# Optimization experiments

Measured on AMD Instinct MI355X. Metric: run time of the kernel, lower is better.

Reference implementation:

```python
import jax, jax.numpy as jnp
import numpy as np

B, N, IN_DIM, D, H, L = 4, 2048, 1, 256, 8, 4
DH = D // H          # 32 head dim
ROPE_D = DH // 2     # 16 = rotary dim per spatial axis (relative_emb_dim=2)
MIN_FREQ_SCALE = 64.0  # scale / min_freq = 1.0 / (1/64)
EPS = 1e-5


def setup_inputs():
    key = jax.random.key(0)
    ks = jax.random.split(key, 12)
    s = 0.02
    return {
        'h': jax.random.normal(ks[0], (B, N, IN_DIM), jnp.float32),
        'pos': jax.random.uniform(ks[1], (B, N, 2), jnp.float32),
        'proj_w': jax.random.normal(ks[2], (IN_DIM, D), jnp.float32) * s,
        'proj_b': jnp.zeros((D,), jnp.float32),
        'qkv_w': jax.random.normal(ks[3], (L, D, 3 * D), jnp.float32) * s,
        'out_w': jax.random.normal(ks[4], (L, D, D), jnp.float32) * s,
        'out_b': jnp.zeros((L, D), jnp.float32),
        'O_w': jax.random.normal(ks[5], (L, D, D), jnp.float32) * s,
        'O_b': jnp.zeros((L, D), jnp.float32),
        'ffn1_w': jax.random.normal(ks[6], (L, D, 2 * D), jnp.float32) * s,
        'ffn1_b': jnp.zeros((L, 2 * D), jnp.float32),
        'ffn2_w': jax.random.normal(ks[7], (L, 2 * D, D), jnp.float32) * s,
        'ffn2_b': jnp.zeros((L, D), jnp.float32),
        'ln1_g': jnp.ones((L, D), jnp.float32),
        'ln1_b': jnp.zeros((L, D), jnp.float32),
        'ln2_g': jnp.ones((L, D), jnp.float32),
        'ln2_b': jnp.zeros((L, D), jnp.float32),
        'final_w': jax.random.normal(ks[8], (D, D), jnp.float32) * s,
    }


def _rope_freqs(coords):
    # coords: (B, N) -> freqs (B, N, ROPE_D)
    inv_freq = 1.0 / (10000.0 ** (jnp.arange(0, ROPE_D, 2, dtype=jnp.float32) / ROPE_D))
    f = (coords * MIN_FREQ_SCALE)[..., None] * inv_freq
    return jnp.concatenate([f, f], axis=-1)


def _rotate_half(x):
    d = x.shape[-1] // 2
    return jnp.concatenate([-x[..., d:], x[..., :d]], axis=-1)


def _apply_rope(t, f):
    return t * jnp.cos(f) + _rotate_half(t) * jnp.sin(f)


def _apply_2d_rope(t, ft, fx):
    d = t.shape[-1] // 2
    return jnp.concatenate([_apply_rope(t[..., :d], ft), _apply_rope(t[..., d:], fx)], axis=-1)


def _ln(x, g, b):
    m = jnp.mean(x, -1, keepdims=True)
    v = jnp.mean((x - m) ** 2, -1, keepdims=True)
    return (x - m) / jnp.sqrt(v + EPS) * g + b


def _forward(h, pos, proj_w, proj_b, qkv_w, out_w, out_b, O_w, O_b,
             ffn1_w, ffn1_b, ffn2_w, ffn2_b, ln1_g, ln1_b, ln2_g, ln2_b, final_w):
    h = h @ proj_w + proj_b                      # (B, N, D)
    ft = _rope_freqs(pos[..., 0])[:, None]       # (B, 1, N, ROPE_D) broadcast over heads
    fx = _rope_freqs(pos[..., 1])[:, None]
    scale = DH ** -0.5
    for l in range(L):
        qkv = h @ qkv_w[l]                       # (B, N, 3D)
        q, k, v = jnp.split(qkv, 3, axis=-1)
        to_heads = lambda t: t.reshape(B, N, H, DH).transpose(0, 2, 1, 3)
        q, k, v = to_heads(q), to_heads(k), to_heads(v)
        q = _apply_2d_rope(q, ft, fx)
        k = _apply_2d_rope(k, ft, fx)
        attn = jax.nn.softmax(jnp.einsum('bhid,bhjd->bhij', q, k) * scale, axis=-1)
        o = jnp.einsum('bhij,bhjd->bhid', attn, v)
        o = o.transpose(0, 2, 1, 3).reshape(B, N, D)
        o = o @ out_w[l] + out_b[l]              # attention to_out
        o = o @ O_w[l] + O_b[l]                  # layer O projection
        h = _ln(h + o, ln1_g[l], ln1_b[l])
        f = jax.nn.relu(h @ ffn1_w[l] + ffn1_b[l]) @ ffn2_w[l] + ffn2_b[l]
        h = _ln(h + f, ln2_g[l], ln2_b[l])
    return h @ final_w


def reference(h, pos, proj_w, proj_b, qkv_w, out_w, out_b, O_w, O_b,
              ffn1_w, ffn1_b, ffn2_w, ffn2_b, ln1_g, ln1_b, ln2_g, ln2_b, final_w):
    return _forward(h, pos, proj_w, proj_b, qkv_w, out_w, out_b, O_w, O_b,
                    ffn1_w, ffn1_b, ffn2_w, ffn2_b, ln1_g, ln1_b, ln2_g, ln2_b, final_w)
```

## Files before the change

### kernel.cpp

```cpp
#include <hip/hip_runtime.h>
#include <math.h>

#define B_ 4
#define N_ 2048
#define D_ 256
#define H_ 8
#define L_ 4
#define DH_ 32

typedef float f32x4 __attribute__((ext_vector_type(4)));
typedef float f32x16 __attribute__((ext_vector_type(16)));
typedef short short8 __attribute__((ext_vector_type(8)));
typedef unsigned short ushort_t;
typedef ushort_t ushortx4 __attribute__((ext_vector_type(4)));
typedef ushort_t ushortx8 __attribute__((ext_vector_type(8)));

typedef __attribute__((address_space(3))) unsigned int lds_u32_t;
typedef __attribute__((address_space(1))) unsigned int glb_u32_t;

static __device__ __forceinline__ ushort_t f2bf(float x) {
    unsigned int u = __float_as_uint(x);
    unsigned int r = (u + 0x7fffu + ((u >> 16) & 1u)) >> 16;
    return (ushort_t)r;
}

static __device__ __forceinline__ unsigned int cvt_pk_bf16(float a, float b) {
    unsigned int w;
    asm("v_cvt_pk_bf16_f32 %0, %1, %2" : "=v"(w) : "v"(a), "v"(b));
    return w;
}

static __device__ __forceinline__ float xhalf_max(float x) {
    unsigned int a = __float_as_uint(x), b = a;
    asm volatile("v_permlane32_swap_b32 %0, %1" : "+v"(a), "+v"(b));
    return fmaxf(__uint_as_float(a), __uint_as_float(b));
}
static __device__ __forceinline__ float xhalf_add(float x) {
    unsigned int a = __float_as_uint(x), b = a;
    asm volatile("v_permlane32_swap_b32 %0, %1" : "+v"(a), "+v"(b));
    return __uint_as_float(a) + __uint_as_float(b);
}

__global__ __launch_bounds__(256) void proj_kernel(
    const float* __restrict__ hin, const float* __restrict__ w,
    const float* __restrict__ bias, float* __restrict__ hout,
    ushort_t* __restrict__ hb)
{
    long idx = (long)blockIdx.x * 256 + threadIdx.x;
    long bn = idx >> 6;
    int d4 = (int)(idx & 63) << 2;
    float hv = hin[bn];
    float4 wv = *(const float4*)&w[d4];
    float4 bv = *(const float4*)&bias[d4];
    float4 o;
    o.x = hv * wv.x + bv.x;
    o.y = hv * wv.y + bv.y;
    o.z = hv * wv.z + bv.z;
    o.w = hv * wv.w + bv.w;
    *(float4*)&hout[bn * D_ + d4] = o;
    ushortx4 ob;
    ob[0] = f2bf(o.x); ob[1] = f2bf(o.y); ob[2] = f2bf(o.z); ob[3] = f2bf(o.w);
    *(ushortx4*)&hb[bn * D_ + d4] = ob;
}

__global__ __launch_bounds__(256) void rope_table_kernel(
    const float* __restrict__ pos, float* __restrict__ tab)
{
    int i = blockIdx.x * 256 + threadIdx.x;
    if (i >= B_ * N_) return;
    float t = pos[i * 2 + 0] * 64.0f;
    float x = pos[i * 2 + 1] * 64.0f;
    float* o = tab + (long)i * 32;
    const float log2_1e4_over8 = 13.28771237954945f / 8.0f;
    #pragma unroll
    for (int j = 0; j < 8; ++j) {
        float invf = exp2f(-(float)j * log2_1e4_over8);
        float st, ct, sx, cx;
        sincosf(t * invf, &st, &ct);
        sincosf(x * invf, &sx, &cx);
        o[j]      = ct;
        o[8 + j]  = st;
        o[16 + j] = cx;
        o[24 + j] = sx;
    }
}

__global__ __launch_bounds__(256) void prep_qkv(
    const float* __restrict__ qkv, const float* __restrict__ tab,
    ushort_t* __restrict__ Qb, ushort_t* __restrict__ Kb, ushort_t* __restrict__ Vt)
{
    const float F = 0.17677669529663687f * 1.4426950408889634f;
    int bh = blockIdx.y;
    int b = bh >> 3, h = bh & 7;
    int n0 = blockIdx.x << 6;
    int t = threadIdx.x;

    #pragma unroll
    for (int i = 0; i < 4; ++i) {
        int item = t + (i << 8);
        int tok = item >> 4, p = item & 15;
        long bn = (long)b * N_ + n0 + tok;
        int half = p >> 3, j = p & 7;
        const float* tb = tab + bn * 32;
        float c = tb[half * 16 + j];
        float s = tb[half * 16 + 8 + j];
        float cF = c * F, sF = s * F;
        long obase = ((long)bh * N_ + n0 + tok) * DH_;
        const float* base = qkv + bn * (3 * D_) + h * DH_ + half * 16 + j;
        int d0 = half * 16 + j;
        float q0 = base[0], q1 = base[8];
        Qb[obase + d0]     = f2bf(q0 * cF - q1 * sF);
        Qb[obase + d0 + 8] = f2bf(q1 * cF + q0 * sF);
        float k0 = base[D_], k1 = base[D_ + 8];
        Kb[obase + d0]     = f2bf(k0 * c - k1 * s);
        Kb[obase + d0 + 8] = f2bf(k1 * c + k0 * s);
    }

    __shared__ float T[64][36];
    int r = t >> 2, c0 = (t & 3) << 3;
    const float* src = qkv + ((long)b * N_ + n0 + r) * (3 * D_) + 2 * D_ + h * DH_ + c0;
    float4 a = ((const float4*)src)[0];
    float4 bb = ((const float4*)src)[1];
    *(float4*)&T[r][c0] = a;
    *(float4*)&T[r][c0 + 4] = bb;
    __syncthreads();
    int d = t >> 3, n8 = (t & 7) << 3;
    ushortx8 o;
    #pragma unroll
    for (int i = 0; i < 8; ++i) o[i] = f2bf(T[n8 + i][d]);
    *(ushortx8*)&Vt[((long)bh * DH_ + d) * N_ + n0 + n8] = o;
}

__global__ __launch_bounds__(256) void wprep_kernel(
    const float* __restrict__ qkv_w, const float* __restrict__ out_w,
    const float* __restrict__ O_w, const float* __restrict__ ffn1_w,
    const float* __restrict__ ffn2_w, const float* __restrict__ final_w,
    ushort_t* __restrict__ WT)
{
    int bid = blockIdx.x;
    const float* src; ushort_t* dst; int K, Nn, tile;
    if (bid < 192)      { int l = bid / 48;        tile = bid % 48;        src = qkv_w  + (long)l * 196608; dst = WT + (long)l * 196608;           K = 256; Nn = 768; }
    else if (bid < 256) { int r = bid - 192; int l = r / 16; tile = r % 16; src = out_w  + (long)l * 65536;  dst = WT + 786432  + (long)l * 65536;  K = 256; Nn = 256; }
    else if (bid < 320) { int r = bid - 256; int l = r / 16; tile = r % 16; src = O_w    + (long)l * 65536;  dst = WT + 1048576 + (long)l * 65536;  K = 256; Nn = 256; }
    else if (bid < 448) { int r = bid - 320; int l = r / 32; tile = r % 32; src = ffn1_w + (long)l * 131072; dst = WT + 1310720 + (long)l * 131072; K = 256; Nn = 512; }
    else if (bid < 576) { int r = bid - 448; int l = r / 32; tile = r % 32; src = ffn2_w + (long)l * 131072; dst = WT + 1835008 + (long)l * 131072; K = 512; Nn = 256; }
    else                { tile = bid - 576;                                 src = final_w;                   dst = WT + 2359296;                    K = 256; Nn = 256; }
    int ntn = Nn >> 6;
    int kt = (tile / ntn) << 6;
    int nt = (tile % ntn) << 6;
    __shared__ float Tl[64][65];
    int t = threadIdx.x;
    int kr = t >> 2, nc0 = (t & 3) << 4;
    const float* sp = src + (long)(kt + kr) * Nn + nt + nc0;
    float4 v0 = ((const float4*)sp)[0];
    float4 v1 = ((const float4*)sp)[1];
    float4 v2 = ((const float4*)sp)[2];
    float4 v3 = ((const float4*)sp)[3];
    float* tr = &Tl[kr][nc0];
    tr[0] = v0.x; tr[1] = v0.y; tr[2] = v0.z; tr[3] = v0.w;
    tr[4] = v1.x; tr[5] = v1.y; tr[6] = v1.z; tr[7] = v1.w;
    tr[8] = v2.x; tr[9] = v2.y; tr[10] = v2.z; tr[11] = v2.w;
    tr[12] = v3.x; tr[13] = v3.y; tr[14] = v3.z; tr[15] = v3.w;
    __syncthreads();
    int n = t >> 2, kc0 = (t & 3) << 4;
    ushortx8 o0, o1;
    #pragma unroll
    for (int i = 0; i < 8; ++i) o0[i] = f2bf(Tl[kc0 + i][n]);
    #pragma unroll
    for (int i = 0; i < 8; ++i) o1[i] = f2bf(Tl[kc0 + 8 + i][n]);
    ushort_t* dp = dst + (long)(nt + n) * K + kt + kc0;
    *(ushortx8*)dp = o0;
    *(ushortx8*)(dp + 8) = o1;
}

__global__ __launch_bounds__(256) void wfold_kernel(
    const float* __restrict__ out_w, const float* __restrict__ O_w,
    ushort_t* __restrict__ WTp)
{
    int l = blockIdx.x >> 4;
    int t4 = blockIdx.x & 15;
    int k0 = (t4 >> 2) << 6, n0 = (t4 & 3) << 6;
    const float* Am = out_w + (long)l * 65536;
    const float* Bm = O_w + (long)l * 65536;
    ushort_t* dst = WTp + (long)l * 65536;
    __shared__ float sA[16][68];
    __shared__ float sB[16][64];
    int tid = threadIdx.x;
    int tx = tid & 15, ty = tid >> 4;
    int arow = tid >> 2, acol = (tid & 3) << 2;
    int brow = tid >> 4, bcol = (tid & 15) << 2;
    const float* Aptr = Am + (long)(k0 + arow) * 256 + acol;
    const float* Bptr = Bm + (long)brow * 256 + n0 + bcol;
    float acc[4][4] = {{0.f}};
    for (int jt = 0; jt < 256; jt += 16) {
        float4 av = *(const float4*)(Aptr + jt);
        float4 bv = *(const float4*)(Bptr + (long)jt * 256);
        __syncthreads();
        sA[acol + 0][arow] = av.x;
        sA[acol + 1][arow] = av.y;
        sA[acol + 2][arow] = av.z;
        sA[acol + 3][arow] = av.w;
        *(float4*)&sB[brow][bcol] = bv;
        __syncthreads();
        #pragma unroll
        for (int kk = 0; kk < 16; ++kk) {
            float4 a = *(const float4*)&sA[kk][ty << 2];
            float4 b = *(const float4*)&sB[kk][tx << 2];
            acc[0][0] += a.x * b.x; acc[0][1] += a.x * b.y; acc[0][2] += a.x * b.z; acc[0][3] += a.x * b.w;
            acc[1][0] += a.y * b.x; acc[1][1] += a.y * b.y; acc[1][2] += a.y * b.z; acc[1][3] += a.y * b.w;
            acc[2][0] += a.z * b.x; acc[2][1] += a.z * b.y; acc[2][2] += a.z * b.z; acc[2][3] += a.z * b.w;
            acc[3][0] += a.w * b.x; acc[3][1] += a.w * b.y; acc[3][2] += a.w * b.z; acc[3][3] += a.w * b.w;
        }
    }
    #pragma unroll
    for (int i = 0; i < 4; ++i) {
        int k = k0 + (ty << 2) + i;
        #pragma unroll
        for (int c = 0; c < 4; ++c) {
            int n = n0 + (tx << 2) + c;
            dst[(long)n * 256 + k] = f2bf(acc[i][c]);
        }
    }
}

__global__ __launch_bounds__(256) void bfold_kernel(
    const float* __restrict__ out_b, const float* __restrict__ O_w,
    const float* __restrict__ O_b, float* __restrict__ bp)
{
    int l = blockIdx.x >> 3;
    int n = ((blockIdx.x & 7) << 5) + (threadIdx.x & 31);
    int jg = threadIdx.x >> 5;
    const float* Bm = O_w + (long)l * 65536;
    float acc = 0.f;
    #pragma unroll 8
    for (int j = jg * 32; j < jg * 32 + 32; ++j)
        acc += out_b[l * 256 + j] * Bm[(long)j * 256 + n];
    __shared__ float red[8][32];
    red[jg][threadIdx.x & 31] = acc;
    __syncthreads();
    if (threadIdx.x < 32) {
        int nn = ((blockIdx.x & 7) << 5) + threadIdx.x;
        float s = O_b[l * 256 + nn];
        #pragma unroll
        for (int g = 0; g < 8; ++g) s += red[g][threadIdx.x];
        bp[l * 256 + nn] = s;
    }
}

__global__ __launch_bounds__(256) void gemm_mfma2(
    const ushort_t* __restrict__ A, const ushort_t* __restrict__ BT,
    const float* __restrict__ bias, void* __restrict__ Cout,
    int N, int K, int flags)
{
    __shared__ ushort_t sA[2][8192];
    __shared__ ushort_t sB[2][4096];
    int tid = threadIdx.x;
    int wid = tid >> 6, lane = tid & 63;
    int lo = lane & 15, hi = lane >> 4;
    int wm = wid >> 1, wn = wid & 1;
    int m0 = blockIdx.y << 7, n0 = blockIdx.x << 6;

    int lrow = lane >> 3;
    int slot = lane & 7;
    const ushort_t* Ag[4];
    const ushort_t* Bg[2];
    #pragma unroll
    for (int c = 0; c < 4; ++c) {
        int arow = (wid << 5) + (c << 3) + lrow;
        Ag[c] = A + (long)(m0 + arow) * K + ((slot ^ lrow) << 3);
    }
    #pragma unroll
    for (int c = 0; c < 2; ++c) {
        int brow = (wid << 4) + (c << 3) + lrow;
        Bg[c] = BT + (long)(n0 + brow) * K + ((slot ^ lrow) << 3);
    }

#define STAGE(buf, koff) do { \
    _Pragma("unroll") \
    for (int c = 0; c < 4; ++c) \
        __builtin_amdgcn_global_load_lds((const glb_u32_t*)(Ag[c] + (koff)), \
            (lds_u32_t*)&sA[buf][((wid << 5) + (c << 3)) << 6], 16, 0, 0); \
    _Pragma("unroll") \
    for (int c = 0; c < 2; ++c) \
        __builtin_amdgcn_global_load_lds((const glb_u32_t*)(Bg[c] + (koff)), \
            (lds_u32_t*)&sB[buf][((wid << 4) + (c << 3)) << 6], 16, 0, 0); \
} while (0)

    f32x4 acc[4][2];
    #pragma unroll
    for (int i = 0; i < 4; ++i)
        #pragma unroll
        for (int j = 0; j < 2; ++j) acc[i][j] = (f32x4){0.f, 0.f, 0.f, 0.f};

    int ar[4], br[2];
    #pragma unroll
    for (int mf = 0; mf < 4; ++mf) ar[mf] = ((wm << 6) + (mf << 4) + lo) << 6;
    #pragma unroll
    for (int nf = 0; nf < 2; ++nf) br[nf] = ((wn << 5) + (nf << 4) + lo) << 6;
    int swz = lo & 7;

    int nk = K >> 6;
    STAGE(0, 0);
    for (int s = 0; s < nk; ++s) {
        int buf = s & 1;
        if (s + 1 < nk) {
            STAGE(buf ^ 1, (s + 1) << 6);
            asm volatile("s_waitcnt vmcnt(6)" ::: "memory");
        } else {
            asm volatile("s_waitcnt vmcnt(0)" ::: "memory");
        }
        __builtin_amdgcn_s_barrier();
        asm volatile("" ::: "memory");
        #pragma unroll
        for (int ks = 0; ks < 2; ++ks) {
            int ko = (((ks << 2) + hi) ^ swz) << 3;
            short8 a0 = *(const short8*)&sA[buf][ar[0] + ko];
            short8 a1 = *(const short8*)&sA[buf][ar[1] + ko];
            short8 a2 = *(const short8*)&sA[buf][ar[2] + ko];
            short8 a3 = *(const short8*)&sA[buf][ar[3] + ko];
            short8 b0 = *(const short8*)&sB[buf][br[0] + ko];
            short8 b1 = *(const short8*)&sB[buf][br[1] + ko];
            acc[0][0] = __builtin_amdgcn_mfma_f32_16x16x32_bf16(a0, b0, acc[0][0], 0, 0, 0);
            acc[0][1] = __builtin_amdgcn_mfma_f32_16x16x32_bf16(a0, b1, acc[0][1], 0, 0, 0);
            acc[1][0] = __builtin_amdgcn_mfma_f32_16x16x32_bf16(a1, b0, acc[1][0], 0, 0, 0);
            acc[1][1] = __builtin_amdgcn_mfma_f32_16x16x32_bf16(a1, b1, acc[1][1], 0, 0, 0);
            acc[2][0] = __builtin_amdgcn_mfma_f32_16x16x32_bf16(a2, b0, acc[2][0], 0, 0, 0);
            acc[2][1] = __builtin_amdgcn_mfma_f32_16x16x32_bf16(a2, b1, acc[2][1], 0, 0, 0);
            acc[3][0] = __builtin_amdgcn_mfma_f32_16x16x32_bf16(a3, b0, acc[3][0], 0, 0, 0);
            acc[3][1] = __builtin_amdgcn_mfma_f32_16x16x32_bf16(a3, b1, acc[3][1], 0, 0, 0);
        }
        asm volatile("" ::: "memory");
        __builtin_amdgcn_s_barrier();
    }
#undef STAGE

    #pragma unroll
    for (int nf = 0; nf < 2; ++nf) {
        int col = n0 + (wn << 5) + (nf << 4) + lo;
        float bv = (flags & 1) ? bias[col] : 0.f;
        #pragma unroll
        for (int mf = 0; mf < 4; ++mf) {
            #pragma unroll
            for (int j = 0; j < 4; ++j) {
                float v = acc[mf][nf][j] + bv;
                if (flags & 2) v = fmaxf(v, 0.f);
                long row = m0 + (wm << 6) + (mf << 4) + (hi << 2) + j;
                if (flags & 4) ((ushort_t*)Cout)[row * N + col] = f2bf(v);
                else           ((float*)Cout)[row * N + col] = v;
            }
        }
    }
}

static __device__ __forceinline__ void attn_tile(
    short8 K00, short8 K01, short8 K10, short8 K11,
    short8 V00, short8 V01, short8 V10, short8 V11,
    short8 qf0, short8 qf1, int half, const f32x16& Z,
    float& m, float& lsum, f32x16& acc)
{
    f32x16 sa = __builtin_amdgcn_mfma_f32_32x32x16_bf16(K00, qf0, Z, 0, 0, 0);
    sa = __builtin_amdgcn_mfma_f32_32x32x16_bf16(K01, qf1, sa, 0, 0, 0);
    f32x16 sb = __builtin_amdgcn_mfma_f32_32x32x16_bf16(K10, qf0, Z, 0, 0, 0);
    sb = __builtin_amdgcn_mfma_f32_32x32x16_bf16(K11, qf1, sb, 0, 0, 0);

    float mx[16];
    #pragma unroll
    for (int r = 0; r < 16; ++r) mx[r] = fmaxf(sa[r], sb[r]);
    #pragma unroll
    for (int st = 8; st >= 1; st >>= 1) {
        #pragma unroll
        for (int r = 0; r < st; ++r) mx[r] = fmaxf(mx[r], mx[r + st]);
    }
    float pmax = xhalf_max(mx[0]);

    if (!__all(pmax <= m + 8.f)) {
        float mn = fmaxf(m, pmax);
        float corr = __builtin_amdgcn_exp2f(m - mn);
        m = mn; lsum *= corr;
        #pragma unroll
        for (int r = 0; r < 16; ++r) {
            int qr = (r & 3) + 8 * (r >> 2) + 4 * half;
            acc[r] *= __shfl(corr, qr, 64);
        }
    }

    float sm[16];
    #pragma unroll
    for (int r = 0; r < 16; ++r) {
        sa[r] = __builtin_amdgcn_exp2f(sa[r] - m);
        sb[r] = __builtin_amdgcn_exp2f(sb[r] - m);
        sm[r] = sa[r] + sb[r];
    }
    #pragma unroll
    for (int st = 8; st >= 1; st >>= 1) {
        #pragma unroll
        for (int r = 0; r < st; ++r) sm[r] += sm[r + st];
    }
    lsum += xhalf_add(sm[0]);

    unsigned int a0 = cvt_pk_bf16(sa[0], sa[1]),   a1 = cvt_pk_bf16(sa[2], sa[3]);
    unsigned int a2 = cvt_pk_bf16(sa[4], sa[5]),   a3 = cvt_pk_bf16(sa[6], sa[7]);
    unsigned int a4 = cvt_pk_bf16(sa[8], sa[9]),   a5 = cvt_pk_bf16(sa[10], sa[11]);
    unsigned int a6 = cvt_pk_bf16(sa[12], sa[13]), a7 = cvt_pk_bf16(sa[14], sa[15]);
    unsigned int b0 = cvt_pk_bf16(sb[0], sb[1]),   b1 = cvt_pk_bf16(sb[2], sb[3]);
    unsigned int b2 = cvt_pk_bf16(sb[4], sb[5]),   b3 = cvt_pk_bf16(sb[6], sb[7]);
    unsigned int b4 = cvt_pk_bf16(sb[8], sb[9]),   b5 = cvt_pk_bf16(sb[10], sb[11]);
    unsigned int b6 = cvt_pk_bf16(sb[12], sb[13]), b7 = cvt_pk_bf16(sb[14], sb[15]);
    asm volatile("v_permlane32_swap_b32 %0, %1" : "+v"(a0), "+v"(a2));
    asm volatile("v_permlane32_swap_b32 %0, %1" : "+v"(a1), "+v"(a3));
    asm volatile("v_permlane32_swap_b32 %0, %1" : "+v"(a4), "+v"(a6));
    asm volatile("v_permlane32_swap_b32 %0, %1" : "+v"(a5), "+v"(a7));
    asm volatile("v_permlane32_swap_b32 %0, %1" : "+v"(b0), "+v"(b2));
    asm volatile("v_permlane32_swap_b32 %0, %1" : "+v"(b1), "+v"(b3));
    asm volatile("v_permlane32_swap_b32 %0, %1" : "+v"(b4), "+v"(b6));
    asm volatile("v_permlane32_swap_b32 %0, %1" : "+v"(b5), "+v"(b7));
    union { unsigned int u[4]; short8 s8; } p0, p1, p2, p3;
    p0.u[0] = a0; p0.u[1] = a1; p0.u[2] = a2; p0.u[3] = a3;
    p1.u[0] = a4; p1.u[1] = a5; p1.u[2] = a6; p1.u[3] = a7;
    p2.u[0] = b0; p2.u[1] = b1; p2.u[2] = b2; p2.u[3] = b3;
    p3.u[0] = b4; p3.u[1] = b5; p3.u[2] = b6; p3.u[3] = b7;
    acc = __builtin_amdgcn_mfma_f32_32x32x16_bf16(p0.s8, V00, acc, 0, 0, 0);
    acc = __builtin_amdgcn_mfma_f32_32x32x16_bf16(p1.s8, V01, acc, 0, 0, 0);
    acc = __builtin_amdgcn_mfma_f32_32x32x16_bf16(p2.s8, V10, acc, 0, 0, 0);
    acc = __builtin_amdgcn_mfma_f32_32x32x16_bf16(p3.s8, V11, acc, 0, 0, 0);
}

__global__ __launch_bounds__(256) void attn_mfma4(
    const ushort_t* __restrict__ Qb, const ushort_t* __restrict__ Kb,
    const ushort_t* __restrict__ Vt, ushort_t* __restrict__ o)
{
    int bh = blockIdx.y;
    int tid = threadIdx.x;
    int wid = tid >> 6, lane = tid & 63;
    int lq = lane & 31;
    int half = lane >> 5;
    int qbase = (blockIdx.x << 7) + wid * 32;

    const ushort_t* Qp = Qb + (long)bh * N_ * DH_;
    const ushort_t* kp = Kb + (long)bh * N_ * DH_ + lq * DH_ + half * 8;
    const ushort_t* vp = Vt + (long)bh * DH_ * N_ + (long)lq * N_ + half * 8;

    short8 qf0 = *(const short8*)&Qp[(long)(qbase + lq) * DH_ + half * 8];
    short8 qf1 = *(const short8*)&Qp[(long)(qbase + lq) * DH_ + 16 + half * 8];

    f32x16 acc, Z;
    #pragma unroll
    for (int r = 0; r < 16; ++r) { acc[r] = 0.f; Z[r] = 0.f; }
    float m = -1e30f, lsum = 0.f;

    short8 k00 = *(const short8*)(kp +  0 * DH_);
    short8 k01 = *(const short8*)(kp +  0 * DH_ + 16);
    short8 k10 = *(const short8*)(kp + 32 * DH_);
    short8 k11 = *(const short8*)(kp + 32 * DH_ + 16);
    short8 v00 = *(const short8*)(vp +  0);
    short8 v01 = *(const short8*)(vp + 16);
    short8 v10 = *(const short8*)(vp + 32);
    short8 v11 = *(const short8*)(vp + 48);

    for (int it = 0; it < N_ / 64 - 1; ++it) {
        long kn = (long)(it + 1) << 6;
        short8 nk00 = *(const short8*)(kp + (kn +  0) * DH_);
        short8 nk01 = *(const short8*)(kp + (kn +  0) * DH_ + 16);
        short8 nk10 = *(const short8*)(kp + (kn + 32) * DH_);
        short8 nk11 = *(const short8*)(kp + (kn + 32) * DH_ + 16);
        short8 nv00 = *(const short8*)(vp + kn);
        short8 nv01 = *(const short8*)(vp + kn + 16);
        short8 nv10 = *(const short8*)(vp + kn + 32);
        short8 nv11 = *(const short8*)(vp + kn + 48);
        attn_tile(k00, k01, k10, k11, v00, v01, v10, v11, qf0, qf1, half, Z, m, lsum, acc);
        k00 = nk00; k01 = nk01; k10 = nk10; k11 = nk11;
        v00 = nv00; v01 = nv01; v10 = nv10; v11 = nv11;
    }
    attn_tile(k00, k01, k10, k11, v00, v01, v10, v11, qf0, qf1, half, Z, m, lsum, acc);

    float invl = 1.f / lsum;
    int b = bh >> 3, h = bh & 7;
    #pragma unroll
    for (int r = 0; r < 16; ++r) {
        int qr = (r & 3) + 8 * (r >> 2) + 4 * half;
        float iv = __shfl(invl, qr, 64);
        long row = (long)b * N_ + qbase + qr;
        o[row * D_ + h * DH_ + lq] = f2bf(acc[r] * iv);
    }
}

__global__ __launch_bounds__(256) void add_ln_kernel(
    float* __restrict__ h, const float* __restrict__ r,
    const float* __restrict__ g, const float* __restrict__ be,
    ushort_t* __restrict__ hb)
{
    int row = blockIdx.x * 4 + (threadIdx.x >> 6);
    int lane = threadIdx.x & 63;
    long off = (long)row * D_ + (lane << 2);
    float4 x = *(float4*)&h[off];
    float4 rr = *(const float4*)&r[off];
    x.x += rr.x; x.y += rr.y; x.z += rr.z; x.w += rr.w;
    float s = x.x + x.y + x.z + x.w;
    #pragma unroll
    for (int k = 1; k < 64; k <<= 1) s += __shfl_xor(s, k, 64);
    float mean = s * (1.f / 256.f);
    float dx = x.x - mean, dy = x.y - mean, dz = x.z - mean, dw = x.w - mean;
    float sq = dx * dx + dy * dy + dz * dz + dw * dw;
    #pragma unroll
    for (int k = 1; k < 64; k <<= 1) sq += __shfl_xor(sq, k, 64);
    float rstd = rsqrtf(sq * (1.f / 256.f) + 1e-5f);
    float4 gv = *(const float4*)&g[lane << 2];
    float4 bv = *(const float4*)&be[lane << 2];
    float4 o;
    o.x = dx * rstd * gv.x + bv.x;
    o.y = dy * rstd * gv.y + bv.y;
    o.z = dz * rstd * gv.z + bv.z;
    o.w = dw * rstd * gv.w + bv.w;
    *(float4*)&h[off] = o;
    ushortx4 ob;
    ob[0] = f2bf(o.x); ob[1] = f2bf(o.y); ob[2] = f2bf(o.z); ob[3] = f2bf(o.w);
    *(ushortx4*)&hb[off] = ob;
}

extern "C" void kernel_launch(void* const* d_in, const int* in_sizes, int n_in,
                              void* d_out, int out_size, void* d_ws, size_t ws_size,
                              hipStream_t stream) {
    const float* h_in    = (const float*)d_in[0];
    const float* pos     = (const float*)d_in[1];
    const float* proj_w  = (const float*)d_in[2];
    const float* proj_b  = (const float*)d_in[3];
    const float* qkv_w   = (const float*)d_in[4];
    const float* out_w   = (const float*)d_in[5];
    const float* out_b   = (const float*)d_in[6];
    const float* O_w     = (const float*)d_in[7];
    const float* O_b     = (const float*)d_in[8];
    const float* ffn1_w  = (const float*)d_in[9];
    const float* ffn1_b  = (const float*)d_in[10];
    const float* ffn2_w  = (const float*)d_in[11];
    const float* ffn2_b  = (const float*)d_in[12];
    const float* ln1_g   = (const float*)d_in[13];
    const float* ln1_b   = (const float*)d_in[14];
    const float* ln2_g   = (const float*)d_in[15];
    const float* ln2_b   = (const float*)d_in[16];
    const float* final_w = (const float*)d_in[17];
    float* out = (float*)d_out;

    float* ws   = (float*)d_ws;
    float* h    = ws;
    float* hb_f = h + 2097152;
    float* tab  = hb_f + 1048576;
    float* WT_f = tab + 262144;
    float* R    = WT_f + 1212416;
    float* QKV  = R + 6291456;
    float* tf   = QKV + 3145728;

    ushort_t* hb  = (ushort_t*)hb_f;
    ushort_t* WT  = (ushort_t*)WT_f;
    float*    qkvf = R;
    ushort_t* aob = (ushort_t*)R;
    ushort_t* fb  = (ushort_t*)(R + 2097152);
    float*    tf32 = R + 4194304;
    ushort_t* Qb  = (ushort_t*)QKV;
    ushort_t* Kb  = Qb + 2097152;
    ushort_t* Vtg = Kb + 2097152;
    ushort_t* WTp = (ushort_t*)tf;
    float*    bp  = tf + 131072;

    const long qkvT_off  = 0;
    const long ffn1T_off = 1310720;
    const long ffn2T_off = 1835008;
    const long finT_off  = 2359296;

    const long M = (long)B_ * N_;

    wprep_kernel<<<592, 256, 0, stream>>>(qkv_w, out_w, O_w, ffn1_w, ffn2_w, final_w, WT);
    wfold_kernel<<<64, 256, 0, stream>>>(out_w, O_w, WTp);
    bfold_kernel<<<32, 256, 0, stream>>>(out_b, O_w, O_b, bp);
    proj_kernel<<<(M * 64) / 256, 256, 0, stream>>>(h_in, proj_w, proj_b, h, hb);
    rope_table_kernel<<<(B_ * N_) / 256, 256, 0, stream>>>(pos, tab);

    for (int l = 0; l < L_; ++l) {
        gemm_mfma2<<<dim3(768 / 64, M / 128), 256, 0, stream>>>(
            hb, WT + qkvT_off + (long)l * 196608, nullptr, qkvf, 768, 256, 0);
        prep_qkv<<<dim3(N_ / 64, B_ * H_), 256, 0, stream>>>(qkvf, tab, Qb, Kb, Vtg);
        attn_mfma4<<<dim3(N_ / 128, B_ * H_), 256, 0, stream>>>(Qb, Kb, Vtg, aob);
        gemm_mfma2<<<dim3(256 / 64, M / 128), 256, 0, stream>>>(
            aob, WTp + (long)l * 65536, bp + (long)l * 256, tf32, 256, 256, 1);
        add_ln_kernel<<<M / 4, 256, 0, stream>>>(
            h, tf32, ln1_g + (long)l * D_, ln1_b + (long)l * D_, hb);
        gemm_mfma2<<<dim3(512 / 64, M / 128), 256, 0, stream>>>(
            hb, WT + ffn1T_off + (long)l * 131072, ffn1_b + (long)l * 2 * D_, fb, 512, 256, 1 | 2 | 4);
        gemm_mfma2<<<dim3(256 / 64, M / 128), 256, 0, stream>>>(
            fb, WT + ffn2T_off + (long)l * 131072, ffn2_b + (long)l * D_, tf32, 256, 512, 1);
        add_ln_kernel<<<M / 4, 256, 0, stream>>>(
            h, tf32, ln2_g + (long)l * D_, ln2_b + (long)l * D_, hb);
    }
    gemm_mfma2<<<dim3(256 / 64, M / 128), 256, 0, stream>>>(
        hb, WT + finT_off, nullptr, out, 256, 256, 0);
}
```

Baseline: 551.4 us.

## Split attention KV range in two with separate combine kernel

Attention now splits the key/value sequence into two halves, each handled by its own block, which doubles the grid from 512 to 1024 blocks to fill more compute units. Each split writes unnormalized fp32 partial outputs plus running max and sum, and a new combine kernel merges them into the bf16 output. The inner tile shrinks from 64 to 32 keys with no register prefetch, and occupancy is hinted through launch_bounds. In exchange it adds fp32 partial-result traffic, an extra kernel launch per layer, and less latency hiding inside the loop.

```diff
diff --git a/kernel.cpp b/kernel.cpp
--- a/kernel.cpp
+++ b/kernel.cpp
@@ -352,22 +352,19 @@
     }
 }
 
-static __device__ __forceinline__ void attn_tile(
-    short8 K00, short8 K01, short8 K10, short8 K11,
-    short8 V00, short8 V01, short8 V10, short8 V11,
+static __device__ __forceinline__ void attn_tile32(
+    short8 kf0, short8 kf1, short8 vb0, short8 vb1,
     short8 qf0, short8 qf1, int half, const f32x16& Z,
     float& m, float& lsum, f32x16& acc)
 {
-    f32x16 sa = __builtin_amdgcn_mfma_f32_32x32x16_bf16(K00, qf0, Z, 0, 0, 0);
-    sa = __builtin_amdgcn_mfma_f32_32x32x16_bf16(K01, qf1, sa, 0, 0, 0);
-    f32x16 sb = __builtin_amdgcn_mfma_f32_32x32x16_bf16(K10, qf0, Z, 0, 0, 0);
-    sb = __builtin_amdgcn_mfma_f32_32x32x16_bf16(K11, qf1, sb, 0, 0, 0);
-
-    float mx[16];
-    #pragma unroll
-    for (int r = 0; r < 16; ++r) mx[r] = fmaxf(sa[r], sb[r]);
-    #pragma unroll
-    for (int st = 8; st >= 1; st >>= 1) {
+    f32x16 sa = __builtin_amdgcn_mfma_f32_32x32x16_bf16(kf0, qf0, Z, 0, 0, 0);
+    sa = __builtin_amdgcn_mfma_f32_32x32x16_bf16(kf1, qf1, sa, 0, 0, 0);
+
+    float mx[8];
+    #pragma unroll
+    for (int r = 0; r < 8; ++r) mx[r] = fmaxf(sa[r], sa[r + 8]);
+    #pragma unroll
+    for (int st = 4; st >= 1; st >>= 1) {
         #pragma unroll
         for (int r = 0; r < st; ++r) mx[r] = fmaxf(mx[r], mx[r + st]);
     }
@@ -384,15 +381,13 @@
         }
     }
 
-    float sm[16];
-    #pragma unroll
-    for (int r = 0; r < 16; ++r) {
-        sa[r] = __builtin_amdgcn_exp2f(sa[r] - m);
-        sb[r] = __builtin_amdgcn_exp2f(sb[r] - m);
-        sm[r] = sa[r] + sb[r];
-    }
-    #pragma unroll
-    for (int st = 8; st >= 1; st >>= 1) {
+    float sm[8];
+    #pragma unroll
+    for (int r = 0; r < 16; ++r) sa[r] = __builtin_amdgcn_exp2f(sa[r] - m);
+    #pragma unroll
+    for (int r = 0; r < 8; ++r) sm[r] = sa[r] + sa[r + 8];
+    #pragma unroll
+    for (int st = 4; st >= 1; st >>= 1) {
         #pragma unroll
         for (int r = 0; r < st; ++r) sm[r] += sm[r + st];
     }
@@ -402,43 +397,33 @@
     unsigned int a2 = cvt_pk_bf16(sa[4], sa[5]),   a3 = cvt_pk_bf16(sa[6], sa[7]);
     unsigned int a4 = cvt_pk_bf16(sa[8], sa[9]),   a5 = cvt_pk_bf16(sa[10], sa[11]);
     unsigned int a6 = cvt_pk_bf16(sa[12], sa[13]), a7 = cvt_pk_bf16(sa[14], sa[15]);
-    unsigned int b0 = cvt_pk_bf16(sb[0], sb[1]),   b1 = cvt_pk_bf16(sb[2], sb[3]);
-    unsigned int b2 = cvt_pk_bf16(sb[4], sb[5]),   b3 = cvt_pk_bf16(sb[6], sb[7]);
-    unsigned int b4 = cvt_pk_bf16(sb[8], sb[9]),   b5 = cvt_pk_bf16(sb[10], sb[11]);
-    unsigned int b6 = cvt_pk_bf16(sb[12], sb[13]), b7 = cvt_pk_bf16(sb[14], sb[15]);
     asm volatile("v_permlane32_swap_b32 %0, %1" : "+v"(a0), "+v"(a2));
     asm volatile("v_permlane32_swap_b32 %0, %1" : "+v"(a1), "+v"(a3));
     asm volatile("v_permlane32_swap_b32 %0, %1" : "+v"(a4), "+v"(a6));
     asm volatile("v_permlane32_swap_b32 %0, %1" : "+v"(a5), "+v"(a7));
-    asm volatile("v_permlane32_swap_b32 %0, %1" : "+v"(b0), "+v"(b2));
-    asm volatile("v_permlane32_swap_b32 %0, %1" : "+v"(b1), "+v"(b3));
-    asm volatile("v_permlane32_swap_b32 %0, %1" : "+v"(b4), "+v"(b6));
-    asm volatile("v_permlane32_swap_b32 %0, %1" : "+v"(b5), "+v"(b7));
-    union { unsigned int u[4]; short8 s8; } p0, p1, p2, p3;
+    union { unsigned int u[4]; short8 s8; } p0, p1;
     p0.u[0] = a0; p0.u[1] = a1; p0.u[2] = a2; p0.u[3] = a3;
     p1.u[0] = a4; p1.u[1] = a5; p1.u[2] = a6; p1.u[3] = a7;
-    p2.u[0] = b0; p2.u[1] = b1; p2.u[2] = b2; p2.u[3] = b3;
-    p3.u[0] = b4; p3.u[1] = b5; p3.u[2] = b6; p3.u[3] = b7;
-    acc = __builtin_amdgcn_mfma_f32_32x32x16_bf16(p0.s8, V00, acc, 0, 0, 0);
-    acc = __builtin_amdgcn_mfma_f32_32x32x16_bf16(p1.s8, V01, acc, 0, 0, 0);
-    acc = __builtin_amdgcn_mfma_f32_32x32x16_bf16(p2.s8, V10, acc, 0, 0, 0);
-    acc = __builtin_amdgcn_mfma_f32_32x32x16_bf16(p3.s8, V11, acc, 0, 0, 0);
-}
-
-__global__ __launch_bounds__(256) void attn_mfma4(
+    acc = __builtin_amdgcn_mfma_f32_32x32x16_bf16(p0.s8, vb0, acc, 0, 0, 0);
+    acc = __builtin_amdgcn_mfma_f32_32x32x16_bf16(p1.s8, vb1, acc, 0, 0, 0);
+}
+
+__global__ __launch_bounds__(256, 4) void attn_split2(
     const ushort_t* __restrict__ Qb, const ushort_t* __restrict__ Kb,
-    const ushort_t* __restrict__ Vt, ushort_t* __restrict__ o)
+    const ushort_t* __restrict__ Vt, float* __restrict__ Op,
+    float2* __restrict__ ml)
 {
     int bh = blockIdx.y;
+    int qt = blockIdx.x & 15, sp = blockIdx.x >> 4;
     int tid = threadIdx.x;
     int wid = tid >> 6, lane = tid & 63;
     int lq = lane & 31;
     int half = lane >> 5;
-    int qbase = (blockIdx.x << 7) + wid * 32;
+    int qbase = (qt << 7) + wid * 32;
 
     const ushort_t* Qp = Qb + (long)bh * N_ * DH_;
-    const ushort_t* kp = Kb + (long)bh * N_ * DH_ + lq * DH_ + half * 8;
-    const ushort_t* vp = Vt + (long)bh * DH_ * N_ + (long)lq * N_ + half * 8;
+    const ushort_t* kp = Kb + (long)bh * N_ * DH_ + ((long)sp << 10) * DH_ + lq * DH_ + half * 8;
+    const ushort_t* vp = Vt + (long)bh * DH_ * N_ + (long)lq * N_ + (sp << 10) + half * 8;
 
     short8 qf0 = *(const short8*)&Qp[(long)(qbase + lq) * DH_ + half * 8];
     short8 qf1 = *(const short8*)&Qp[(long)(qbase + lq) * DH_ + 16 + half * 8];
@@ -448,40 +433,59 @@
     for (int r = 0; r < 16; ++r) { acc[r] = 0.f; Z[r] = 0.f; }
     float m = -1e30f, lsum = 0.f;
 
-    short8 k00 = *(const short8*)(kp +  0 * DH_);
-    short8 k01 = *(const short8*)(kp +  0 * DH_ + 16);
-    short8 k10 = *(const short8*)(kp + 32 * DH_);
-    short8 k11 = *(const short8*)(kp + 32 * DH_ + 16);
-    short8 v00 = *(const short8*)(vp +  0);
-    short8 v01 = *(const short8*)(vp + 16);
-    short8 v10 = *(const short8*)(vp + 32);
-    short8 v11 = *(const short8*)(vp + 48);
-
-    for (int it = 0; it < N_ / 64 - 1; ++it) {
-        long kn = (long)(it + 1) << 6;
-        short8 nk00 = *(const short8*)(kp + (kn +  0) * DH_);
-        short8 nk01 = *(const short8*)(kp + (kn +  0) * DH_ + 16);
-        short8 nk10 = *(const short8*)(kp + (kn + 32) * DH_);
-        short8 nk11 = *(const short8*)(kp + (kn + 32) * DH_ + 16);
-        short8 nv00 = *(const short8*)(vp + kn);
-        short8 nv01 = *(const short8*)(vp + kn + 16);
-        short8 nv10 = *(const short8*)(vp + kn + 32);
-        short8 nv11 = *(const short8*)(vp + kn + 48);
-        attn_tile(k00, k01, k10, k11, v00, v01, v10, v11, qf0, qf1, half, Z, m, lsum, acc);
-        k00 = nk00; k01 = nk01; k10 = nk10; k11 = nk11;
-        v00 = nv00; v01 = nv01; v10 = nv10; v11 = nv11;
-    }
-    attn_tile(k00, k01, k10, k11, v00, v01, v10, v11, qf0, qf1, half, Z, m, lsum, acc);
-
-    float invl = 1.f / lsum;
-    int b = bh >> 3, h = bh & 7;
+    #pragma unroll 1
+    for (int it = 0; it < 1024 / 32; ++it) {
+        long k0 = (long)it << 5;
+        short8 kf0 = *(const short8*)(kp + k0 * DH_);
+        short8 kf1 = *(const short8*)(kp + k0 * DH_ + 16);
+        short8 vb0 = *(const short8*)(vp + k0);
+        short8 vb1 = *(const short8*)(vp + k0 + 16);
+        attn_tile32(kf0, kf1, vb0, vb1, qf0, qf1, half, Z, m, lsum, acc);
+    }
+
+    float* OpB = Op + (long)sp * 2097152;
+    float2* mlB = ml + (long)sp * 65536;
     #pragma unroll
     for (int r = 0; r < 16; ++r) {
         int qr = (r & 3) + 8 * (r >> 2) + 4 * half;
-        float iv = __shfl(invl, qr, 64);
-        long row = (long)b * N_ + qbase + qr;
-        o[row * D_ + h * DH_ + lq] = f2bf(acc[r] * iv);
-    }
+        long row = (long)bh * N_ + qbase + qr;
+        OpB[row * 32 + lq] = acc[r];
+    }
+    if (lane < 32) mlB[(long)bh * N_ + qbase + lq] = make_float2(m, lsum);
+}
+
+__global__ __launch_bounds__(256) void attn_combine(
+    const float* __restrict__ Op, const float2* __restrict__ ml,
+    ushort_t* __restrict__ o)
+{
+    int i = blockIdx.x * 256 + threadIdx.x;
+    int bh = i >> 11, q = i & 2047;
+    int b = bh >> 3, h = bh & 7;
+    float2 m0 = ml[i];
+    float2 m1 = ml[65536 + i];
+    float mn = fmaxf(m0.x, m1.x);
+    float c0 = __builtin_amdgcn_exp2f(m0.x - mn);
+    float c1 = __builtin_amdgcn_exp2f(m1.x - mn);
+    float inv = 1.f / (c0 * m0.y + c1 * m1.y);
+    float f0 = c0 * inv, f1 = c1 * inv;
+    const f32x4* O0 = (const f32x4*)(Op + (long)i * 32);
+    const f32x4* O1 = (const f32x4*)(Op + 2097152 + (long)i * 32);
+    unsigned int w[16];
+    #pragma unroll
+    for (int v = 0; v < 8; ++v) {
+        f32x4 a = O0[v], bb = O1[v];
+        float e0 = f0 * a[0] + f1 * bb[0];
+        float e1 = f0 * a[1] + f1 * bb[1];
+        float e2 = f0 * a[2] + f1 * bb[2];
+        float e3 = f0 * a[3] + f1 * bb[3];
+        w[2 * v]     = cvt_pk_bf16(e0, e1);
+        w[2 * v + 1] = cvt_pk_bf16(e2, e3);
+    }
+    uint4* dst = (uint4*)&o[((long)b * N_ + q) * D_ + h * DH_];
+    dst[0] = make_uint4(w[0], w[1], w[2], w[3]);
+    dst[1] = make_uint4(w[4], w[5], w[6], w[7]);
+    dst[2] = make_uint4(w[8], w[9], w[10], w[11]);
+    dst[3] = make_uint4(w[12], w[13], w[14], w[15]);
 }
 
 __global__ __launch_bounds__(256) void add_ln_kernel(
@@ -553,6 +557,7 @@
     ushort_t* WT  = (ushort_t*)WT_f;
     float*    qkvf = R;
     ushort_t* aob = (ushort_t*)R;
+    float*    Op  = R + 2097152;
     ushort_t* fb  = (ushort_t*)(R + 2097152);
     float*    tf32 = R + 4194304;
     ushort_t* Qb  = (ushort_t*)QKV;
@@ -560,6 +565,7 @@
     ushort_t* Vtg = Kb + 2097152;
     ushort_t* WTp = (ushort_t*)tf;
     float*    bp  = tf + 131072;
+    float2*   mlb = (float2*)(tf + 262144);
 
     const long qkvT_off  = 0;
     const long ffn1T_off = 1310720;
@@ -578,7 +584,8 @@
         gemm_mfma2<<<dim3(768 / 64, M / 128), 256, 0, stream>>>(
             hb, WT + qkvT_off + (long)l * 196608, nullptr, qkvf, 768, 256, 0);
         prep_qkv<<<dim3(N_ / 64, B_ * H_), 256, 0, stream>>>(qkvf, tab, Qb, Kb, Vtg);
-        attn_mfma4<<<dim3(N_ / 128, B_ * H_), 256, 0, stream>>>(Qb, Kb, Vtg, aob);
+        attn_split2<<<dim3(32, B_ * H_), 256, 0, stream>>>(Qb, Kb, Vtg, Op, mlb);
+        attn_combine<<<256, 256, 0, stream>>>(Op, mlb, aob);
         gemm_mfma2<<<dim3(256 / 64, M / 128), 256, 0, stream>>>(
             aob, WTp + (long)l * 65536, bp + (long)l * 256, tf32, 256, 256, 1);
         add_ln_kernel<<<M / 4, 256, 0, stream>>>(
```

Result: slower. 592.6 us (+7.5%).
